# Optimization experiments

Measured on AMD Instinct MI355X. Metric: run time of the kernel, lower is better.

Reference implementation:

```python
import jax, jax.numpy as jnp
import numpy as np

K = 3        # kernel_size
STRIDE = 1
PAD = 1
DIL = 1


def setup_inputs() -> dict:
    key = jax.random.key(0)
    k1, k2, k3 = jax.random.split(key, 3)
    B, C, H, W = 8, 256, 64, 64
    O = 256
    x = jax.random.normal(k1, (B, C, H, W), jnp.float32)
    # offset conv: Conv2d(C, 2*K*K, K, stride, pad) with bias
    w_off = jax.random.normal(k2, (2 * K * K, C, K, K), jnp.float32) * 0.01
    b_off = jnp.zeros((2 * K * K,), jnp.float32)
    # DeformConv weight (mmcv DeformConv has no bias)
    w_dcn = jax.random.normal(k3, (O, C, K, K), jnp.float32) * (1.0 / np.sqrt(C * K * K))
    return {"x": x, "w_off": w_off, "b_off": b_off, "w_dcn": w_dcn}


def _conv(x, w):
    return jax.lax.conv_general_dilated(
        x, w, window_strides=(STRIDE, STRIDE),
        padding=[(PAD, PAD), (PAD, PAD)], rhs_dilation=(DIL, DIL),
        dimension_numbers=("NCHW", "OIHW", "NCHW"))


def _bilinear(img_flat, y, x, H, W):
    # img_flat: [C, H*W]; y, x: [KK, Ho, Wo] float sampling coords
    y0 = jnp.floor(y)
    x0 = jnp.floor(x)
    out = jnp.zeros((img_flat.shape[0],) + y.shape, img_flat.dtype)
    for dy in (0.0, 1.0):
        for dx in (0.0, 1.0):
            yi = y0 + dy
            xi = x0 + dx
            wgt = (1.0 - jnp.abs(y - yi)) * (1.0 - jnp.abs(x - xi))
            valid = (yi >= 0) & (yi < H) & (xi >= 0) & (xi < W)
            yc = jnp.clip(yi, 0, H - 1).astype(jnp.int32)
            xc = jnp.clip(xi, 0, W - 1).astype(jnp.int32)
            idx = yc * W + xc                       # [KK,Ho,Wo]
            g = jnp.take(img_flat, idx.reshape(-1), axis=1)
            g = g.reshape((img_flat.shape[0],) + y.shape)  # [C,KK,Ho,Wo]
            out = out + g * (wgt * valid)[None]
    return out


def reference(x, w_off, b_off, w_dcn):
    B, C, H, W = x.shape
    O = w_dcn.shape[0]
    # 1) predict offsets: [B, 2*K*K, Ho, Wo], channel order (ky,kx) pairs per tap
    offset = _conv(x, w_off) + b_off[None, :, None, None]
    Ho, Wo = offset.shape[2], offset.shape[3]
    off = offset.reshape(B, K * K, 2, Ho, Wo)
    off_y = off[:, :, 0]   # [B,KK,Ho,Wo]
    off_x = off[:, :, 1]
    # 2) base sampling grid for a standard conv
    ky, kx = jnp.meshgrid(jnp.arange(K), jnp.arange(K), indexing="ij")
    ky = ky.reshape(-1).astype(x.dtype)   # [KK]
    kx = kx.reshape(-1).astype(x.dtype)
    hy = (jnp.arange(Ho) * STRIDE - PAD).astype(x.dtype)
    wx = (jnp.arange(Wo) * STRIDE - PAD).astype(x.dtype)
    base_y = hy[None, :, None] + (ky * DIL)[:, None, None]  # [KK,Ho,1]
    base_x = wx[None, None, :] + (kx * DIL)[:, None, None]  # [KK,1,Wo]
    sy = off_y + base_y[None]   # [B,KK,Ho,Wo]
    sx = off_x + base_x[None]
    # 3) bilinear gather: sampled patches [B,C,KK,Ho,Wo]
    img_flat = x.reshape(B, C, H * W)
    sampled = jax.vmap(lambda im, yy, xx: _bilinear(im, yy, xx, H, W))(img_flat, sy, sx)
    # 4) weighted sum over (C, kernel taps)
    out = jnp.einsum("bckhw,ock->bohw", sampled, w_dcn.reshape(O, C, K * K))
    return out
```

## Files before the change

kernel.cpp:

```cpp
#include <hip/hip_runtime.h>
#include <hip/hip_bf16.h>


#define HW 64
#define CCH 256
#define OCH 256
#define BB 8
#define KDIM 2304

typedef __attribute__((ext_vector_type(8))) short bf16x8;
typedef __attribute__((ext_vector_type(8))) unsigned short u16x8;
typedef __attribute__((ext_vector_type(4))) float f32x4;
typedef __attribute__((ext_vector_type(2))) float f32x2;
typedef __attribute__((ext_vector_type(4))) unsigned short u16x4;
typedef __attribute__((ext_vector_type(4))) unsigned int u32x4;

static __device__ inline unsigned short f2bf(float f) {
  unsigned u = __builtin_bit_cast(unsigned, f);
  u += 0x7FFFu + ((u >> 16) & 1u);
  return (unsigned short)(u >> 16);
}
static __device__ inline float bf2f(unsigned short s) {
  return __builtin_bit_cast(float, (unsigned)s << 16);
}
static __device__ inline unsigned cvt_pk_bf16(float lo, float hi) {
  unsigned r;
  asm("v_cvt_pk_bf16_f32 %0, %1, %2" : "=v"(r) : "v"(lo), "v"(hi));
  return r;
}

#define GLL16(gsrc, ldst)                                                      \
  __builtin_amdgcn_global_load_lds(                                           \
      (const __attribute__((address_space(1))) void*)(gsrc),                  \
      (__attribute__((address_space(3))) void*)(ldst), 16, 0, 0)

static __device__ inline int xcd_swz256(int bid) {
  return (bid & 7) * 32 + (bid >> 3);
}

__global__ __launch_bounds__(256) void prep_xpose(
    const float* __restrict__ x, const float* __restrict__ w_dcn,
    const float* __restrict__ w_off, unsigned short* __restrict__ xTbf,
    unsigned short* __restrict__ W2, unsigned short* __restrict__ Wop,
    unsigned short* __restrict__ zp) {
  const int tid = threadIdx.x;
  const int bid = blockIdx.x;
  if (bid < 2048) {
    __shared__ float t[64][65];
    const int ct = bid & 3;
    const int pt = (bid >> 2) & 63;
    const int b = bid >> 8;
#pragma unroll
    for (int i = 0; i < 16; ++i) {
      int cl = i * 4 + (tid >> 6);
      int p = tid & 63;
      t[cl][p] = x[(((b << 8) + ct * 64 + cl) << 12) + pt * 64 + p];
    }
    __syncthreads();
#pragma unroll
    for (int i = 0; i < 4; ++i) {
      int pl = i * 16 + (tid >> 4);
      int c4 = (tid & 15) * 4;
      u16x4 v;
      v[0] = f2bf(t[c4][pl]);
      v[1] = f2bf(t[c4 + 1][pl]);
      v[2] = f2bf(t[c4 + 2][pl]);
      v[3] = f2bf(t[c4 + 3][pl]);
      *(u16x4*)(xTbf + (((size_t)((b << 12) + pt * 64 + pl)) << 8) + ct * 64 +
                c4) = v;
    }
  } else {
    int i = (bid - 2048) * 256 + tid;
    if (i < 9 * 256 * 256) {
      int o = i / KDIM;
      int r = i - o * KDIM;
      int kk = r >> 8, c = r & 255;
      W2[i] = f2bf(w_dcn[((o << 8) + c) * 9 + kk]);
    }
    if (i < 32 * KDIM) {
      int n = i / KDIM;
      int r = i - n * KDIM;
      int kk = r >> 8, c = r & 255;
      Wop[i] = (n < 18) ? f2bf(w_off[((n << 8) + c) * 9 + kk]) : (unsigned short)0;
    }
    if (i < 512) zp[i] = 0;
  }
}

__global__ __launch_bounds__(512) void offset_gemm(
    const unsigned short* __restrict__ xTbf, const unsigned short* __restrict__ Wop,
    const unsigned short* __restrict__ zp, const float* __restrict__ b_off,
    float* __restrict__ off_buf) {
  __shared__ short ldsA[2][128 * 64];
  __shared__ short ldsB[2][32 * 64];
  const int tid = threadIdx.x;
  const int lane = tid & 63;
  const int wid = __builtin_amdgcn_readfirstlane(tid >> 6);
  const int m0 = xcd_swz256(blockIdx.x) * 128;
  const int b = m0 >> 12;
  const unsigned short* xb = xTbf + ((size_t)b << 20);

  int hA[2], wA2[2], scA[2], dstA[2];
#pragma unroll
  for (int g = 0; g < 2; ++g) {
    const int idx = g * 512 + tid;
    const int r = idx >> 3, c = idx & 7;
    const int pos = (m0 & 4095) + r;
    hA[g] = pos >> 6;
    wA2[g] = pos & 63;
    scA[g] = ((c ^ (r & 7)) << 3);
    dstA[g] = idx * 8;
  }
  const int rBs = tid >> 3;
  const unsigned short* srcB =
      Wop + (size_t)rBs * KDIM + (((tid & 7) ^ (rBs & 7)) << 3);

  const int l15 = lane & 15, l4 = lane >> 4;
  const int rA = wid * 16 + l15;
  int offA[2], offB[2][2];
#pragma unroll
  for (int h = 0; h < 2; ++h) {
    offA[h] = rA * 64 + (((h * 4 + l4) ^ (rA & 7)) << 3);
#pragma unroll
    for (int f = 0; f < 2; ++f) {
      const int rb = f * 16 + l15;
      offB[f][h] = rb * 64 + (((h * 4 + l4) ^ (rb & 7)) << 3);
    }
  }

  const f32x4 z = {0.f, 0.f, 0.f, 0.f};
  f32x4 acc[2];
  acc[0] = z;
  acc[1] = z;

  auto stage = [&](int buf, int t) {
    const int tap = t >> 2;
    const int c0 = (t & 3) * 64;
    const int dy = tap / 3 - 1, dx = tap - (tap / 3) * 3 - 1;
#pragma unroll
    for (int g = 0; g < 2; ++g) {
      const int y = hA[g] + dy, xx = wA2[g] + dx;
      const bool valid = ((unsigned)y < 64u) && ((unsigned)xx < 64u);
      const unsigned short* src =
          valid ? xb + ((((y << 6) + xx) << 8) + c0 + scA[g]) : zp + scA[g];
      GLL16(src, &ldsA[buf][dstA[g]]);
    }
    if (tid < 256) GLL16(srcB + t * 64, &ldsB[buf][tid * 8]);
  };

  stage(0, 0);
  __syncthreads();

  for (int t = 0; t < 36; ++t) {
    const int buf = t & 1;
    if (t < 35) stage(buf ^ 1, t + 1);
#pragma unroll
    for (int h = 0; h < 2; ++h) {
      bf16x8 af = *(const bf16x8*)&ldsA[buf][offA[h]];
      bf16x8 bfr[2];
#pragma unroll
      for (int f = 0; f < 2; ++f) bfr[f] = *(const bf16x8*)&ldsB[buf][offB[f][h]];
#pragma unroll
      for (int j = 0; j < 2; ++j)
        acc[j] = __builtin_amdgcn_mfma_f32_16x16x32_bf16(af, bfr[j], acc[j],
                                                         0, 0, 0);
    }
    __syncthreads();
  }

#pragma unroll
  for (int j = 0; j < 2; ++j) {
    const int col = j * 16 + l15;
    if (col < 18) {
      const float bias = b_off[col];
#pragma unroll
      for (int rr = 0; rr < 4; ++rr) {
        const int m = m0 + wid * 16 + l4 * 4 + rr;
        off_buf[(size_t)m * 18 + col] = acc[j][rr] + bias;
      }
    }
  }
}

__global__ __launch_bounds__(512, 2) void dcn_fused(
    const unsigned short* __restrict__ xTbf, const float* __restrict__ off_buf,
    const unsigned short* __restrict__ W2, float* __restrict__ out) {
  __shared__ f32x2 slyx[128][9];
  __shared__ u16x4 spos[128][9];
  __shared__ short ldsA[2][128 * 64];
  __shared__ short ldsB[2][256 * 64];

  const int tid = threadIdx.x;
  const int lane = tid & 63;
  const int wid = __builtin_amdgcn_readfirstlane(tid >> 6);
  const int m0 = xcd_swz256(blockIdx.x) * 128;
  const int b = m0 >> 12;
  const unsigned short* xb = xTbf + ((size_t)b << 20);

  for (int idx = tid; idx < 128 * 9; idx += 512) {
    const int r = idx / 9, k = idx - (idx / 9) * 9;
    const int ky = k / 3, kx = k - ky * 3;
    const int pos = (m0 & 4095) + r;
    const int h = pos >> 6, w = pos & 63;
    const float offy = off_buf[(size_t)(m0 + r) * 18 + 2 * k];
    const float offx = off_buf[(size_t)(m0 + r) * 18 + 2 * k + 1];
    const float sy = offy + (float)(h - 1 + ky);
    const float sx = offx + (float)(w - 1 + kx);
    const float y0f = floorf(sy), x0f = floorf(sx);
    const int y0 = (int)y0f, x0 = (int)x0f;
    const int y1 = y0 + 1, x1 = x0 + 1;
    const unsigned vy0 = ((unsigned)y0 < 64u), vy1 = ((unsigned)y1 < 64u);
    const unsigned vx0 = ((unsigned)x0 < 64u), vx1 = ((unsigned)x1 < 64u);
    const int y0c = min(max(y0, 0), HW - 1), y1c = min(max(y1, 0), HW - 1);
    const int x0c = min(max(x0, 0), HW - 1), x1c = min(max(x1, 0), HW - 1);
    f32x2 lyx;
    lyx[0] = sy - y0f;
    lyx[1] = sx - x0f;
    u16x4 pp;
    pp[0] = (unsigned short)(((y0c << 6) + x0c) | ((vy0 & vx0) << 15));
    pp[1] = (unsigned short)(((y0c << 6) + x1c) | ((vy0 & vx1) << 15));
    pp[2] = (unsigned short)(((y1c << 6) + x0c) | ((vy1 & vx0) << 15));
    pp[3] = (unsigned short)(((y1c << 6) + x1c) | ((vy1 & vx1) << 15));
    slyx[r][k] = lyx;
    spos[r][k] = pp;
  }

  const int r = tid >> 2, q = tid & 3;
  const int dstA0 = r * 64 + (((2 * q) ^ (r & 7)) << 3);
  const int dstA1 = r * 64 + (((2 * q + 1) ^ (r & 7)) << 3);

  const unsigned short* srcBp[4];
  int dstB[4];
#pragma unroll
  for (int g = 0; g < 4; ++g) {
    const int idx = g * 512 + tid;
    const int row = idx >> 3, c = idx & 7;
    srcBp[g] = W2 + (size_t)row * KDIM + ((c ^ (row & 7)) << 3);
    dstB[g] = idx * 8;
  }

  const int l15 = lane & 15, l4 = lane >> 4;
  const int wm = wid & 1, wn = wid >> 1;
  int offA[4][2], offB[4][2];
#pragma unroll
  for (int f = 0; f < 4; ++f) {
    const int rA = wm * 64 + f * 16 + l15;
    const int rB = wn * 64 + f * 16 + l15;
#pragma unroll
    for (int h = 0; h < 2; ++h) {
      offA[f][h] = rA * 64 + (((h * 4 + l4) ^ (rA & 7)) << 3);
      offB[f][h] = rB * 64 + (((h * 4 + l4) ^ (rB & 7)) << 3);
    }
  }

  const f32x4 z = {0.f, 0.f, 0.f, 0.f};
  f32x4 acc[4][4];
#pragma unroll
  for (int i = 0; i < 4; ++i)
#pragma unroll
    for (int j = 0; j < 4; ++j) acc[i][j] = z;

  __syncthreads();

  f32x4 wv;
  int av[4];
  auto load_params = [&](int tap) {
    const f32x2 lyx = slyx[r][tap];
    const u16x4 pp = spos[r][tap];
    const float ly = lyx[0], lx = lyx[1];
#pragma unroll
    for (int e = 0; e < 4; ++e) av[e] = (int)(pp[e] & 0x0FFFu) << 8;
    wv[0] = (1.f - ly) * (1.f - lx) * (float)(pp[0] >> 15);
    wv[1] = (1.f - ly) * lx * (float)(pp[1] >> 15);
    wv[2] = ly * (1.f - lx) * (float)(pp[2] >> 15);
    wv[3] = ly * lx * (float)(pp[3] >> 15);
  };

  u16x8 gc0[2], gc1[2], gc2[2], gc3[2];
  f32x4 gw;

  auto issue_gathers = [&](int t) {
    const int cb = ((t & 3) << 6) + q * 16;
#pragma unroll
    for (int h = 0; h < 2; ++h) {
      gc0[h] = *(const u16x8*)(xb + av[0] + cb + h * 8);
      gc1[h] = *(const u16x8*)(xb + av[1] + cb + h * 8);
      gc2[h] = *(const u16x8*)(xb + av[2] + cb + h * 8);
      gc3[h] = *(const u16x8*)(xb + av[3] + cb + h * 8);
    }
    gw = wv;
  };

  auto lerp_store = [&](int buf) {
    short* base = ldsA[buf];
#pragma unroll
    for (int h = 0; h < 2; ++h) {
      u32x4 wds;
#pragma unroll
      for (int e = 0; e < 4; ++e) {
        const float f0 = gw[0] * bf2f(gc0[h][2 * e]) + gw[1] * bf2f(gc1[h][2 * e]) +
                         gw[2] * bf2f(gc2[h][2 * e]) + gw[3] * bf2f(gc3[h][2 * e]);
        const float f1 = gw[0] * bf2f(gc0[h][2 * e + 1]) +
                         gw[1] * bf2f(gc1[h][2 * e + 1]) +
                         gw[2] * bf2f(gc2[h][2 * e + 1]) +
                         gw[3] * bf2f(gc3[h][2 * e + 1]);
        wds[e] = cvt_pk_bf16(f0, f1);
      }
      *(u32x4*)&base[h == 0 ? dstA0 : dstA1] = wds;
    }
  };

  load_params(0);
  issue_gathers(0);
  lerp_store(0);
#pragma unroll
  for (int g = 0; g < 4; ++g) GLL16(srcBp[g], &ldsB[0][dstB[g]]);
  __syncthreads();

  for (int t = 0; t < 36; ++t) {
    const int buf = t & 1;
    if (t < 35) {
      const int tn = t + 1;
#pragma unroll
      for (int g = 0; g < 4; ++g) GLL16(srcBp[g] + tn * 64, &ldsB[buf ^ 1][dstB[g]]);
      if ((tn & 3) == 0) load_params(tn >> 2);
      issue_gathers(tn);
    }
#pragma unroll
    for (int h = 0; h < 2; ++h) {
      bf16x8 af[4], bfr[4];
#pragma unroll
      for (int f = 0; f < 4; ++f) {
        af[f] = *(const bf16x8*)&ldsA[buf][offA[f][h]];
        bfr[f] = *(const bf16x8*)&ldsB[buf][offB[f][h]];
      }
#pragma unroll
      for (int i = 0; i < 4; ++i)
#pragma unroll
        for (int j = 0; j < 4; ++j)
          acc[i][j] = __builtin_amdgcn_mfma_f32_16x16x32_bf16(af[i], bfr[j],
                                                              acc[i][j], 0, 0, 0);
    }
    if (t < 35) lerp_store(buf ^ 1);
    __syncthreads();
  }

#pragma unroll
  for (int i = 0; i < 4; ++i) {
    const int m = m0 + wm * 64 + i * 16 + l4 * 4;
    const int bb = m >> 12;
    const int pos = m & 4095;
#pragma unroll
    for (int j = 0; j < 4; ++j) {
      const int o = wn * 64 + j * 16 + l15;
      *(f32x4*)(out + (((size_t)bb * OCH + o) << 12) + pos) = acc[i][j];
    }
  }
}

extern "C" void kernel_launch(void* const* d_in, const int* in_sizes, int n_in,
                              void* d_out, int out_size, void* d_ws,
                              size_t ws_size, hipStream_t stream) {
  const float* x = (const float*)d_in[0];
  const float* w_off = (const float*)d_in[1];
  const float* b_off = (const float*)d_in[2];
  const float* w_dcn = (const float*)d_in[3];
  float* out = (float*)d_out;

  char* ws = (char*)d_ws;
  float* off_buf = (float*)(ws);
  unsigned short* Wop = (unsigned short*)(ws + 2359296);
  unsigned short* zp = (unsigned short*)(ws + 2506752);
  unsigned short* W2 = (unsigned short*)(ws + 2507776);
  unsigned short* xTbf = (unsigned short*)(ws + 3687424);

  prep_xpose<<<4352, 256, 0, stream>>>(x, w_dcn, w_off, xTbf, W2, Wop, zp);
  offset_gemm<<<256, 512, 0, stream>>>(xTbf, Wop, zp, b_off, off_buf);
  dcn_fused<<<256, 512, 0, stream>>>(xTbf, off_buf, W2, out);
}
```

Measured before the change: 114.6 us.

## Fuse offset-prediction GEMM into DCN kernel and pack bilinear lerp math

Merges the offset conv GEMM into the main deformable-conv kernel so each block computes its own 128 rows of offsets into shared memory. This removes a kernel launch and the global round trip through off_buf. It also rewrites the bilinear interpolation to use packed v_pk_mul/v_pk_fma f32 ops on pairs of unpacked bf16 values, cutting VALU instruction count. The cost is higher register and LDS pressure in the fused kernel, and the offset phase now runs serially inside each block before the main loop.

```diff
diff --git a/kernel.cpp b/kernel.cpp
--- a/kernel.cpp
+++ b/kernel.cpp
@@ -20,12 +20,25 @@
   u += 0x7FFFu + ((u >> 16) & 1u);
   return (unsigned short)(u >> 16);
 }
-static __device__ inline float bf2f(unsigned short s) {
-  return __builtin_bit_cast(float, (unsigned)s << 16);
-}
 static __device__ inline unsigned cvt_pk_bf16(float lo, float hi) {
   unsigned r;
   asm("v_cvt_pk_bf16_f32 %0, %1, %2" : "=v"(r) : "v"(lo), "v"(hi));
+  return r;
+}
+static __device__ inline f32x2 pk_mul_f32(f32x2 a, f32x2 b) {
+  f32x2 d;
+  asm("v_pk_mul_f32 %0, %1, %2" : "=v"(d) : "v"(a), "v"(b));
+  return d;
+}
+static __device__ inline f32x2 pk_fma_f32(f32x2 a, f32x2 b, f32x2 c) {
+  f32x2 d;
+  asm("v_pk_fma_f32 %0, %1, %2, %3" : "=v"(d) : "v"(a), "v"(b), "v"(c));
+  return d;
+}
+static __device__ inline f32x2 unpk_bf16(unsigned p) {
+  f32x2 r;
+  r[0] = __builtin_bit_cast(float, p << 16);
+  r[1] = __builtin_bit_cast(float, p & 0xFFFF0000u);
   return r;
 }
 
@@ -87,123 +100,113 @@
   }
 }
 
-__global__ __launch_bounds__(512) void offset_gemm(
+__global__ __launch_bounds__(512, 2) void dcn_fused(
     const unsigned short* __restrict__ xTbf, const unsigned short* __restrict__ Wop,
     const unsigned short* __restrict__ zp, const float* __restrict__ b_off,
-    float* __restrict__ off_buf) {
+    const unsigned short* __restrict__ W2, float* __restrict__ out) {
+  __shared__ float soff[128][18];
+  __shared__ f32x2 slyx[128][9];
+  __shared__ u16x4 spos[128][9];
   __shared__ short ldsA[2][128 * 64];
-  __shared__ short ldsB[2][32 * 64];
+  __shared__ short ldsB[2][256 * 64];
+
   const int tid = threadIdx.x;
   const int lane = tid & 63;
   const int wid = __builtin_amdgcn_readfirstlane(tid >> 6);
   const int m0 = xcd_swz256(blockIdx.x) * 128;
   const int b = m0 >> 12;
   const unsigned short* xb = xTbf + ((size_t)b << 20);
-
-  int hA[2], wA2[2], scA[2], dstA[2];
-#pragma unroll
-  for (int g = 0; g < 2; ++g) {
-    const int idx = g * 512 + tid;
-    const int r = idx >> 3, c = idx & 7;
-    const int pos = (m0 & 4095) + r;
-    hA[g] = pos >> 6;
-    wA2[g] = pos & 63;
-    scA[g] = ((c ^ (r & 7)) << 3);
-    dstA[g] = idx * 8;
-  }
-  const int rBs = tid >> 3;
-  const unsigned short* srcB =
-      Wop + (size_t)rBs * KDIM + (((tid & 7) ^ (rBs & 7)) << 3);
-
   const int l15 = lane & 15, l4 = lane >> 4;
-  const int rA = wid * 16 + l15;
-  int offA[2], offB[2][2];
-#pragma unroll
-  for (int h = 0; h < 2; ++h) {
-    offA[h] = rA * 64 + (((h * 4 + l4) ^ (rA & 7)) << 3);
-#pragma unroll
-    for (int f = 0; f < 2; ++f) {
-      const int rb = f * 16 + l15;
-      offB[f][h] = rb * 64 + (((h * 4 + l4) ^ (rb & 7)) << 3);
-    }
-  }
-
   const f32x4 z = {0.f, 0.f, 0.f, 0.f};
-  f32x4 acc[2];
-  acc[0] = z;
-  acc[1] = z;
-
-  auto stage = [&](int buf, int t) {
-    const int tap = t >> 2;
-    const int c0 = (t & 3) * 64;
-    const int dy = tap / 3 - 1, dx = tap - (tap / 3) * 3 - 1;
+
+  {
+    int phA[2], pwA[2], pscA[2], pdstA[2];
 #pragma unroll
     for (int g = 0; g < 2; ++g) {
-      const int y = hA[g] + dy, xx = wA2[g] + dx;
-      const bool valid = ((unsigned)y < 64u) && ((unsigned)xx < 64u);
-      const unsigned short* src =
-          valid ? xb + ((((y << 6) + xx) << 8) + c0 + scA[g]) : zp + scA[g];
-      GLL16(src, &ldsA[buf][dstA[g]]);
-    }
-    if (tid < 256) GLL16(srcB + t * 64, &ldsB[buf][tid * 8]);
-  };
-
-  stage(0, 0);
-  __syncthreads();
-
-  for (int t = 0; t < 36; ++t) {
-    const int buf = t & 1;
-    if (t < 35) stage(buf ^ 1, t + 1);
-#pragma unroll
-    for (int h = 0; h < 2; ++h) {
-      bf16x8 af = *(const bf16x8*)&ldsA[buf][offA[h]];
-      bf16x8 bfr[2];
-#pragma unroll
-      for (int f = 0; f < 2; ++f) bfr[f] = *(const bf16x8*)&ldsB[buf][offB[f][h]];
-#pragma unroll
-      for (int j = 0; j < 2; ++j)
-        acc[j] = __builtin_amdgcn_mfma_f32_16x16x32_bf16(af, bfr[j], acc[j],
-                                                         0, 0, 0);
-    }
+      const int idx = g * 512 + tid;
+      const int pr = idx >> 3, pc = idx & 7;
+      const int pos = (m0 & 4095) + pr;
+      phA[g] = pos >> 6;
+      pwA[g] = pos & 63;
+      pscA[g] = ((pc ^ (pr & 7)) << 3);
+      pdstA[g] = idx * 8;
+    }
+    const int rBs = tid >> 3;
+    const unsigned short* srcB =
+        Wop + (size_t)rBs * KDIM + (((tid & 7) ^ (rBs & 7)) << 3);
+
+    const int rA = wid * 16 + l15;
+    int offAp[2], offBp[2][2];
+#pragma unroll
+    for (int h = 0; h < 2; ++h) {
+      offAp[h] = rA * 64 + (((h * 4 + l4) ^ (rA & 7)) << 3);
+#pragma unroll
+      for (int f = 0; f < 2; ++f) {
+        const int rb = f * 16 + l15;
+        offBp[f][h] = rb * 64 + (((h * 4 + l4) ^ (rb & 7)) << 3);
+      }
+    }
+
+    f32x4 pacc[2];
+    pacc[0] = z;
+    pacc[1] = z;
+
+    auto stage = [&](int buf, int t) {
+      const int tap = t >> 2;
+      const int c0 = (t & 3) * 64;
+      const int dy = tap / 3 - 1, dx = tap - (tap / 3) * 3 - 1;
+#pragma unroll
+      for (int g = 0; g < 2; ++g) {
+        const int y = phA[g] + dy, xx = pwA[g] + dx;
+        const bool valid = ((unsigned)y < 64u) && ((unsigned)xx < 64u);
+        const unsigned short* src =
+            valid ? xb + ((((y << 6) + xx) << 8) + c0 + pscA[g]) : zp + pscA[g];
+        GLL16(src, &ldsA[buf][pdstA[g]]);
+      }
+      if (tid < 256) GLL16(srcB + t * 64, &ldsB[buf][tid * 8]);
+    };
+
+    stage(0, 0);
     __syncthreads();
-  }
-
-#pragma unroll
-  for (int j = 0; j < 2; ++j) {
-    const int col = j * 16 + l15;
-    if (col < 18) {
-      const float bias = b_off[col];
-#pragma unroll
-      for (int rr = 0; rr < 4; ++rr) {
-        const int m = m0 + wid * 16 + l4 * 4 + rr;
-        off_buf[(size_t)m * 18 + col] = acc[j][rr] + bias;
-      }
-    }
-  }
-}
-
-__global__ __launch_bounds__(512, 2) void dcn_fused(
-    const unsigned short* __restrict__ xTbf, const float* __restrict__ off_buf,
-    const unsigned short* __restrict__ W2, float* __restrict__ out) {
-  __shared__ f32x2 slyx[128][9];
-  __shared__ u16x4 spos[128][9];
-  __shared__ short ldsA[2][128 * 64];
-  __shared__ short ldsB[2][256 * 64];
-
-  const int tid = threadIdx.x;
-  const int lane = tid & 63;
-  const int wid = __builtin_amdgcn_readfirstlane(tid >> 6);
-  const int m0 = xcd_swz256(blockIdx.x) * 128;
-  const int b = m0 >> 12;
-  const unsigned short* xb = xTbf + ((size_t)b << 20);
+
+    for (int t = 0; t < 36; ++t) {
+      const int buf = t & 1;
+      if (t < 35) stage(buf ^ 1, t + 1);
+#pragma unroll
+      for (int h = 0; h < 2; ++h) {
+        bf16x8 af = *(const bf16x8*)&ldsA[buf][offAp[h]];
+        bf16x8 bfr[2];
+#pragma unroll
+        for (int f = 0; f < 2; ++f)
+          bfr[f] = *(const bf16x8*)&ldsB[buf][offBp[f][h]];
+#pragma unroll
+        for (int j = 0; j < 2; ++j)
+          pacc[j] = __builtin_amdgcn_mfma_f32_16x16x32_bf16(af, bfr[j],
+                                                            pacc[j], 0, 0, 0);
+      }
+      __syncthreads();
+    }
+
+#pragma unroll
+    for (int j = 0; j < 2; ++j) {
+      const int col = j * 16 + l15;
+      if (col < 18) {
+        const float bias = b_off[col];
+#pragma unroll
+        for (int rr = 0; rr < 4; ++rr)
+          soff[wid * 16 + l4 * 4 + rr][col] = pacc[j][rr] + bias;
+      }
+    }
+    __syncthreads();
+  }
 
   for (int idx = tid; idx < 128 * 9; idx += 512) {
     const int r = idx / 9, k = idx - (idx / 9) * 9;
     const int ky = k / 3, kx = k - ky * 3;
     const int pos = (m0 & 4095) + r;
     const int h = pos >> 6, w = pos & 63;
-    const float offy = off_buf[(size_t)(m0 + r) * 18 + 2 * k];
-    const float offx = off_buf[(size_t)(m0 + r) * 18 + 2 * k + 1];
+    const float offy = soff[r][2 * k];
+    const float offx = soff[r][2 * k + 1];
     const float sy = offy + (float)(h - 1 + ky);
     const float sx = offx + (float)(w - 1 + kx);
     const float y0f = floorf(sy), x0f = floorf(sx);
@@ -239,7 +242,6 @@
     dstB[g] = idx * 8;
   }
 
-  const int l15 = lane & 15, l4 = lane >> 4;
   const int wm = wid & 1, wn = wid >> 1;
   int offA[4][2], offB[4][2];
 #pragma unroll
@@ -253,7 +255,6 @@
     }
   }
 
-  const f32x4 z = {0.f, 0.f, 0.f, 0.f};
   f32x4 acc[4][4];
 #pragma unroll
   for (int i = 0; i < 4; ++i)
@@ -262,7 +263,7 @@
 
   __syncthreads();
 
-  f32x4 wv;
+  f32x2 wpk[4];
   int av[4];
   auto load_params = [&](int tap) {
     const f32x2 lyx = slyx[r][tap];
@@ -270,14 +271,20 @@
     const float ly = lyx[0], lx = lyx[1];
 #pragma unroll
     for (int e = 0; e < 4; ++e) av[e] = (int)(pp[e] & 0x0FFFu) << 8;
-    wv[0] = (1.f - ly) * (1.f - lx) * (float)(pp[0] >> 15);
-    wv[1] = (1.f - ly) * lx * (float)(pp[1] >> 15);
-    wv[2] = ly * (1.f - lx) * (float)(pp[2] >> 15);
-    wv[3] = ly * lx * (float)(pp[3] >> 15);
+    float wf[4];
+    wf[0] = (1.f - ly) * (1.f - lx) * (float)(pp[0] >> 15);
+    wf[1] = (1.f - ly) * lx * (float)(pp[1] >> 15);
+    wf[2] = ly * (1.f - lx) * (float)(pp[2] >> 15);
+    wf[3] = ly * lx * (float)(pp[3] >> 15);
+#pragma unroll
+    for (int e = 0; e < 4; ++e) {
+      wpk[e][0] = wf[e];
+      wpk[e][1] = wf[e];
+    }
   };
 
   u16x8 gc0[2], gc1[2], gc2[2], gc3[2];
-  f32x4 gw;
+  f32x2 gwpk[4];
 
   auto issue_gathers = [&](int t) {
     const int cb = ((t & 3) << 6) + q * 16;
@@ -288,23 +295,26 @@
       gc2[h] = *(const u16x8*)(xb + av[2] + cb + h * 8);
       gc3[h] = *(const u16x8*)(xb + av[3] + cb + h * 8);
     }
-    gw = wv;
+#pragma unroll
+    for (int e = 0; e < 4; ++e) gwpk[e] = wpk[e];
   };
 
   auto lerp_store = [&](int buf) {
     short* base = ldsA[buf];
 #pragma unroll
     for (int h = 0; h < 2; ++h) {
+      const u32x4 c0 = __builtin_bit_cast(u32x4, gc0[h]);
+      const u32x4 c1 = __builtin_bit_cast(u32x4, gc1[h]);
+      const u32x4 c2 = __builtin_bit_cast(u32x4, gc2[h]);
+      const u32x4 c3 = __builtin_bit_cast(u32x4, gc3[h]);
       u32x4 wds;
 #pragma unroll
       for (int e = 0; e < 4; ++e) {
-        const float f0 = gw[0] * bf2f(gc0[h][2 * e]) + gw[1] * bf2f(gc1[h][2 * e]) +
-                         gw[2] * bf2f(gc2[h][2 * e]) + gw[3] * bf2f(gc3[h][2 * e]);
-        const float f1 = gw[0] * bf2f(gc0[h][2 * e + 1]) +
-                         gw[1] * bf2f(gc1[h][2 * e + 1]) +
-                         gw[2] * bf2f(gc2[h][2 * e + 1]) +
-                         gw[3] * bf2f(gc3[h][2 * e + 1]);
-        wds[e] = cvt_pk_bf16(f0, f1);
+        f32x2 s = pk_mul_f32(unpk_bf16(c0[e]), gwpk[0]);
+        s = pk_fma_f32(unpk_bf16(c1[e]), gwpk[1], s);
+        s = pk_fma_f32(unpk_bf16(c2[e]), gwpk[2], s);
+        s = pk_fma_f32(unpk_bf16(c3[e]), gwpk[3], s);
+        wds[e] = cvt_pk_bf16(s[0], s[1]);
       }
       *(u32x4*)&base[h == 0 ? dstA0 : dstA1] = wds;
     }
@@ -368,13 +378,11 @@
   float* out = (float*)d_out;
 
   char* ws = (char*)d_ws;
-  float* off_buf = (float*)(ws);
   unsigned short* Wop = (unsigned short*)(ws + 2359296);
   unsigned short* zp = (unsigned short*)(ws + 2506752);
   unsigned short* W2 = (unsigned short*)(ws + 2507776);
   unsigned short* xTbf = (unsigned short*)(ws + 3687424);
 
   prep_xpose<<<4352, 256, 0, stream>>>(x, w_dcn, w_off, xTbf, W2, Wop, zp);
-  offset_gemm<<<256, 512, 0, stream>>>(xTbf, Wop, zp, b_off, off_buf);
-  dcn_fused<<<256, 512, 0, stream>>>(xTbf, off_buf, W2, out);
-}
+  dcn_fused<<<256, 512, 0, stream>>>(xTbf, Wop, zp, b_off, W2, out);
+}
```

After: 105.6 us. -7.8%, faster.
